# Kernel optimization log

Measured on AMD Instinct MI355X. Metric: run time of the kernel, lower is better.

The kernel has to match this reference:

```python
import jax, jax.numpy as jnp
import numpy as np

B, S, H = 8, 2048, 768
N_SPANS = 512
MAX_SPAN_LEN = 30
WIDTH_VOCAB = 64
N_BIO, N_TYPE, N_SENS = 3, 18, 4
SPAN_DIM = H * 3 + H // 2  # 2688


def setup_inputs() -> dict:
    key = jax.random.key(0)
    ks = jax.random.split(key, 12)
    hidden = jax.random.normal(ks[0], (B, S, H), dtype=jnp.float32)
    # candidate spans: start in [0, S-MAX_SPAN_LEN), width in [1, MAX_SPAN_LEN]
    starts = jax.random.randint(ks[1], (B, N_SPANS), 0, S - MAX_SPAN_LEN)
    widths = jax.random.randint(ks[2], (B, N_SPANS), 1, MAX_SPAN_LEN + 1)
    ends = starts + widths - 1
    candidate_spans = jnp.stack([starts, ends], axis=-1).astype(jnp.int32)  # [B,N,2]
    sc = 0.02
    return {
        "hidden": hidden,
        "candidate_spans": candidate_spans,
        "width_emb": jax.random.normal(ks[3], (WIDTH_VOCAB, H // 2), dtype=jnp.float32) * sc,
        "W_prop": jax.random.normal(ks[4], (H, N_BIO), dtype=jnp.float32) * sc,
        "b_prop": jnp.zeros((N_BIO,), jnp.float32),
        "W_t1": jax.random.normal(ks[5], (SPAN_DIM, H), dtype=jnp.float32) * sc,
        "b_t1": jnp.zeros((H,), jnp.float32),
        "W_t2": jax.random.normal(ks[6], (H, N_TYPE), dtype=jnp.float32) * sc,
        "b_t2": jnp.zeros((N_TYPE,), jnp.float32),
        "W_s1": jax.random.normal(ks[7], (SPAN_DIM + N_TYPE, H), dtype=jnp.float32) * sc,
        "b_s1": jnp.zeros((H,), jnp.float32),
        "W_s2": jax.random.normal(ks[8], (H, N_SENS), dtype=jnp.float32) * sc,
        "b_s2": jnp.zeros((N_SENS,), jnp.float32),
    }


def _span_reprs(hidden, candidate_spans, width_emb):
    # hidden: [B,S,H], candidate_spans: [B,N,2] (all spans valid, 0 <= s <= e < S)
    starts = candidate_spans[..., 0]  # [B,N]
    ends = candidate_spans[..., 1]    # [B,N]
    gather = jax.vmap(lambda h, i: h[i])  # per-batch row gather
    start_h = gather(hidden, starts)  # [B,N,H]
    end_h = gather(hidden, ends)      # [B,N,H]
    # ragged mean-pool via inclusive prefix sums: sum(h[s:e+1]) = P[e+1]-P[s]
    P = jnp.concatenate(
        [jnp.zeros((hidden.shape[0], 1, hidden.shape[2]), hidden.dtype),
         jnp.cumsum(hidden, axis=1)], axis=1)  # [B,S+1,H]
    widths = ends - starts + 1  # [B,N]
    pooled = (gather(P, ends + 1) - gather(P, starts)) / widths[..., None].astype(hidden.dtype)
    width_h = width_emb[jnp.clip(widths, None, WIDTH_VOCAB - 1)]  # [B,N,H//2]
    return jnp.concatenate([start_h, end_h, pooled, width_h], axis=-1)  # [B,N,SPAN_DIM]


def reference(hidden, candidate_spans, width_emb, W_prop, b_prop,
              W_t1, b_t1, W_t2, b_t2, W_s1, b_s1, W_s2, b_s2):
    # proposal head (dropout = identity in eval)
    proposal_logits = hidden @ W_prop + b_prop  # [B,S,3]
    rep = _span_reprs(hidden, candidate_spans, width_emb)  # [B,N,2688]
    t = jax.nn.gelu(rep @ W_t1 + b_t1, approximate=False)
    type_logits = t @ W_t2 + b_t2  # [B,N,18]
    type_probs = jax.nn.softmax(type_logits, axis=-1)
    s_in = jnp.concatenate([rep, type_probs], axis=-1)  # [B,N,2706]
    s = jax.nn.gelu(s_in @ W_s1 + b_s1, approximate=False)
    sensitivity_logits = s @ W_s2 + b_s2  # [B,N,4]
    return proposal_logits, type_logits, sensitivity_logits
```

## Files before the change

### kernel.cpp

```cpp
#include <hip/hip_runtime.h>
#include <hip/hip_bf16.h>
#include <math.h>

#define Bn 8
#define Sn 2048
#define Hn 768
#define NROW 4096
#define SPAN_DIM 2688
#define NBIG 1536
#define NTYPE 18
#define NSENS 4

typedef __attribute__((ext_vector_type(8))) short short8;
typedef __attribute__((ext_vector_type(4))) float floatx4;

__device__ __forceinline__ unsigned short f2bf(float x) {
    __hip_bfloat16 h = __float2bfloat16(x);
    return *reinterpret_cast<unsigned short*>(&h);
}

__device__ __forceinline__ void glds16(const void* g, void* l) {
    __builtin_amdgcn_global_load_lds(
        (const __attribute__((address_space(1))) unsigned int*)g,
        (__attribute__((address_space(3))) unsigned int*)l, 16, 0, 0);
}

__device__ __forceinline__ float gelu_exact(float v) {
    return 0.5f * v * (1.f + erff(v * 0.70710678118654752f));
}

__global__ __launch_bounds__(256) void proposal_kernel(
    const float* __restrict__ hidden, const float* __restrict__ Wp,
    const float* __restrict__ bp, float* __restrict__ out)
{
    int wave = threadIdx.x >> 6;
    int lane = threadIdx.x & 63;
    int row  = blockIdx.x * 4 + wave;
    const float4* h4 = (const float4*)(hidden + (size_t)row * Hn);
    float a0 = 0.f, a1 = 0.f, a2 = 0.f;
#pragma unroll
    for (int i = 0; i < 3; ++i) {
        int kc = i * 64 + lane;
        float4 h = h4[kc];
        const float* w = Wp + kc * 12;
        a0 += h.x * w[0] + h.y * w[3] + h.z * w[6] + h.w * w[9];
        a1 += h.x * w[1] + h.y * w[4] + h.z * w[7] + h.w * w[10];
        a2 += h.x * w[2] + h.y * w[5] + h.z * w[8] + h.w * w[11];
    }
#pragma unroll
    for (int off = 32; off; off >>= 1) {
        a0 += __shfl_xor(a0, off);
        a1 += __shfl_xor(a1, off);
        a2 += __shfl_xor(a2, off);
    }
    if (lane < 3) {
        float v = (lane == 0 ? a0 : (lane == 1 ? a1 : a2)) + bp[lane];
        out[row * 3 + lane] = v;
    }
}

__global__ __launch_bounds__(192) void span_rep_kernel(
    const float* __restrict__ hidden, const int* __restrict__ spans,
    const float* __restrict__ wemb, unsigned short* __restrict__ rep)
{
    int n = blockIdx.x;
    int b = n >> 9;
    int s = spans[n * 2 + 0];
    int e = spans[n * 2 + 1];
    int w = e - s + 1;
    const float4* hb4 = (const float4*)(hidden + (size_t)b * Sn * Hn);
    unsigned short* r = rep + (size_t)n * SPAN_DIM;
    float inv_w = 1.0f / (float)w;
    int tid = threadIdx.x;

    float4 sv = hb4[(size_t)s * 192 + tid];
    float4 ev = hb4[(size_t)e * 192 + tid];
    float4 pv = make_float4(0.f, 0.f, 0.f, 0.f);
    for (int rr = s; rr <= e; ++rr) {
        float4 h = hb4[(size_t)rr * 192 + tid];
        pv.x += h.x; pv.y += h.y; pv.z += h.z; pv.w += h.w;
    }
    pv.x *= inv_w; pv.y *= inv_w; pv.z *= inv_w; pv.w *= inv_w;

    *(ushort4*)&r[tid * 4] =
        make_ushort4(f2bf(sv.x), f2bf(sv.y), f2bf(sv.z), f2bf(sv.w));
    *(ushort4*)&r[Hn + tid * 4] =
        make_ushort4(f2bf(ev.x), f2bf(ev.y), f2bf(ev.z), f2bf(ev.w));
    *(ushort4*)&r[2 * Hn + tid * 4] =
        make_ushort4(f2bf(pv.x), f2bf(pv.y), f2bf(pv.z), f2bf(pv.w));
    if (tid < 96) {
        int wi = w > 63 ? 63 : w;
        float4 wv = ((const float4*)wemb)[wi * 96 + tid];
        *(ushort4*)&r[3 * Hn + tid * 4] =
            make_ushort4(f2bf(wv.x), f2bf(wv.y), f2bf(wv.z), f2bf(wv.w));
    }
}

__global__ __launch_bounds__(256) void transpose_cvt(
    const float* __restrict__ W, unsigned short* __restrict__ Wt,
    int Kin, int N, int ldt)
{
    __shared__ float tile[32][33];
    int k0 = blockIdx.x * 32;
    int n0 = blockIdx.y * 32;
    int tx = threadIdx.x & 31, ty = threadIdx.x >> 5;
#pragma unroll
    for (int i = 0; i < 32; i += 8) {
        int k = k0 + ty + i;
        tile[ty + i][tx] = (k < Kin) ? W[(size_t)k * N + n0 + tx] : 0.f;
    }
    __syncthreads();
#pragma unroll
    for (int i = 0; i < 32; i += 8) {
        int nn = n0 + ty + i;
        Wt[(size_t)nn * ldt + k0 + tx] = f2bf(tile[tx][ty + i]);
    }
}

__global__ __launch_bounds__(256, 3) void gemm_fused(
    const unsigned short* __restrict__ A,
    const unsigned short* __restrict__ Bt,
    const float* __restrict__ bt1, const float* __restrict__ bs1,
    float* __restrict__ obuf)
{
    const int BM = 128, BN = 64, BK = 32;
    __shared__ unsigned short As[BM * BK];
    __shared__ unsigned short Bs[BN * BK];

    int tid = threadIdx.x, wave = tid >> 6, lane = tid & 63;
    int m0 = blockIdx.x * BM, n0 = blockIdx.y * BN;

    int wr = (wave >> 1) * 64;
    int wc = (wave & 1) * 32;
    int fr = lane & 15;
    int fc = lane >> 4;

    int rA0 = tid >> 2,        cA0 = (tid & 3) ^ ((rA0 >> 1) & 3);
    int dA1 = 256 + tid;
    int rA1 = dA1 >> 2,        cA1 = (dA1 & 3) ^ ((rA1 >> 1) & 3);
    int rB  = tid >> 2,        cB  = (tid & 3) ^ ((rB >> 1) & 3);

    const unsigned short* gA0 = A + (size_t)(m0 + rA0) * SPAN_DIM + cA0 * 8;
    const unsigned short* gA1 = A + (size_t)(m0 + rA1) * SPAN_DIM + cA1 * 8;
    const unsigned short* gB  = Bt + (size_t)(n0 + rB) * SPAN_DIM + cB * 8;

    unsigned short* ldsA0 = As + wave * 512;
    unsigned short* ldsA1 = As + 2048 + wave * 512;
    unsigned short* ldsB  = Bs + wave * 512;

    floatx4 acc[4][2] = {};

    for (int k0 = 0; k0 < SPAN_DIM; k0 += BK) {
        glds16(gA0 + k0, ldsA0);
        glds16(gA1 + k0, ldsA1);
        glds16(gB + k0, ldsB);
        __syncthreads();

        short8 af[4], bf[2];
#pragma unroll
        for (int i = 0; i < 4; ++i) {
            int r = wr + i * 16 + fr;
            af[i] = *(const short8*)&As[(r * 4 + (fc ^ ((r >> 1) & 3))) * 8];
        }
#pragma unroll
        for (int i = 0; i < 2; ++i) {
            int r = wc + i * 16 + fr;
            bf[i] = *(const short8*)&Bs[(r * 4 + (fc ^ ((r >> 1) & 3))) * 8];
        }
#pragma unroll
        for (int mi = 0; mi < 4; ++mi)
#pragma unroll
            for (int ni = 0; ni < 2; ++ni)
                acc[mi][ni] = __builtin_amdgcn_mfma_f32_16x16x32_bf16(
                    af[mi], bf[ni], acc[mi][ni], 0, 0, 0);
        __syncthreads();
    }

    bool isT = (n0 < Hn);
    const float* bias = isT ? bt1 : (bs1 - Hn);
    int cr = (lane >> 4) * 4;
#pragma unroll
    for (int mi = 0; mi < 4; ++mi) {
#pragma unroll
        for (int ni = 0; ni < 2; ++ni) {
            int col = n0 + wc + ni * 16 + fr;
            float bv = bias[col];
#pragma unroll
            for (int r = 0; r < 4; ++r) {
                int row = m0 + wr + mi * 16 + cr + r;
                float v = acc[mi][ni][r] + bv;
                if (isT) v = gelu_exact(v);
                obuf[(size_t)row * NBIG + col] = v;
            }
        }
    }
}

__global__ __launch_bounds__(64) void type_head_kernel(
    const float* __restrict__ obuf, const float* __restrict__ W2,
    const float* __restrict__ b2, float* __restrict__ logits_out,
    float* __restrict__ pbuf)
{
    int row = blockIdx.x;
    int lane = threadIdx.x;
    const float* tr = obuf + (size_t)row * NBIG;
    float acc[NTYPE] = {};
#pragma unroll
    for (int i = 0; i < Hn / 64; ++i) {
        int k = lane + i * 64;
        float tv = tr[k];
        const float* wk = W2 + k * NTYPE;
#pragma unroll
        for (int o = 0; o < NTYPE; ++o) acc[o] += tv * wk[o];
    }
#pragma unroll
    for (int o = 0; o < NTYPE; ++o)
#pragma unroll
        for (int off = 32; off; off >>= 1) acc[o] += __shfl_xor(acc[o], off);

    float mx = -1e30f;
#pragma unroll
    for (int o = 0; o < NTYPE; ++o) { acc[o] += b2[o]; mx = fmaxf(mx, acc[o]); }
    float p[NTYPE];
    float sum = 0.f;
#pragma unroll
    for (int o = 0; o < NTYPE; ++o) { p[o] = expf(acc[o] - mx); sum += p[o]; }
    float inv = 1.f / sum;
    if (lane < NTYPE) {
        logits_out[row * NTYPE + lane] = acc[lane];
        pbuf[row * NTYPE + lane] = p[lane] * inv;
    }
}

__global__ __launch_bounds__(64) void tail_sens_kernel(
    const float* __restrict__ obuf, const float* __restrict__ pbuf,
    const float* __restrict__ Ws1, const float* __restrict__ Ws2,
    const float* __restrict__ bs2, float* __restrict__ out)
{
    int row = blockIdx.x;
    int lane = threadIdx.x;
    const float* sp = obuf + (size_t)row * NBIG + Hn;
    float pr[NTYPE];
#pragma unroll
    for (int o = 0; o < NTYPE; ++o) pr[o] = pbuf[row * NTYPE + o];
    float acc[NSENS] = {};
#pragma unroll
    for (int i = 0; i < 12; ++i) {
        int j = lane + i * 64;
        float v = sp[j];
        float t = 0.f;
#pragma unroll
        for (int o = 0; o < NTYPE; ++o)
            t += pr[o] * Ws1[(size_t)(SPAN_DIM + o) * Hn + j];
        v = gelu_exact(v + t);
#pragma unroll
        for (int o = 0; o < NSENS; ++o) acc[o] += v * Ws2[j * NSENS + o];
    }
#pragma unroll
    for (int o = 0; o < NSENS; ++o)
#pragma unroll
        for (int off = 32; off; off >>= 1) acc[o] += __shfl_xor(acc[o], off);
    if (lane < NSENS) out[row * NSENS + lane] = acc[lane] + bs2[lane];
}

extern "C" void kernel_launch(void* const* d_in, const int* in_sizes, int n_in,
                              void* d_out, int out_size, void* d_ws, size_t ws_size,
                              hipStream_t stream)
{
    const float* hidden = (const float*)d_in[0];
    const int*   spans  = (const int*)d_in[1];
    const float* wemb   = (const float*)d_in[2];
    const float* Wp     = (const float*)d_in[3];
    const float* bp     = (const float*)d_in[4];
    const float* Wt1    = (const float*)d_in[5];
    const float* bt1    = (const float*)d_in[6];
    const float* Wt2    = (const float*)d_in[7];
    const float* bt2    = (const float*)d_in[8];
    const float* Ws1    = (const float*)d_in[9];
    const float* bs1    = (const float*)d_in[10];
    const float* Ws2    = (const float*)d_in[11];
    const float* bs2    = (const float*)d_in[12];

    float* out      = (float*)d_out;
    float* out_prop = out;
    float* out_type = out + Bn * Sn * 3;
    float* out_sens = out_type + NROW * NTYPE;

    unsigned short* rep = (unsigned short*)d_ws;
    float* obuf = (float*)(rep + (size_t)NROW * SPAN_DIM);
    unsigned short* WbigT = (unsigned short*)(obuf + (size_t)NROW * NBIG);
    float* pbuf = (float*)(WbigT + (size_t)NBIG * SPAN_DIM);

    transpose_cvt<<<dim3(SPAN_DIM / 32, Hn / 32), 256, 0, stream>>>(
        Wt1, WbigT, SPAN_DIM, Hn, SPAN_DIM);
    transpose_cvt<<<dim3(SPAN_DIM / 32, Hn / 32), 256, 0, stream>>>(
        Ws1, WbigT + (size_t)Hn * SPAN_DIM, SPAN_DIM, Hn, SPAN_DIM);

    proposal_kernel<<<Bn * Sn / 4, 256, 0, stream>>>(hidden, Wp, bp, out_prop);
    span_rep_kernel<<<NROW, 192, 0, stream>>>(hidden, spans, wemb, rep);

    dim3 gg(NROW / 128, NBIG / 64);
    gemm_fused<<<gg, 256, 0, stream>>>(rep, WbigT, bt1, bs1, obuf);

    type_head_kernel<<<NROW, 64, 0, stream>>>(obuf, Wt2, bt2, out_type, pbuf);
    tail_sens_kernel<<<NROW, 64, 0, stream>>>(obuf, pbuf, Ws1, Ws2, bs2, out_sens);
}
```

Baseline: 241.8 us.

## Fuse head kernels, merge weight prep, double GEMM K-tile, unroll span pooling

Merges the two weight transpose launches into one prep kernel that also transposes the small head weights for coalesced access. Fuses the type head and sensitivity tail into one kernel with four rows per block, dropping the probability buffer round trip. Raises the GEMM K-tile from 32 to 64 with a wider swizzle so fewer barriers are paid per K step, at the cost of double the LDS. Unrolls the span mean-pool loop by four with independent accumulators to raise memory-level parallelism.

```diff
diff --git a/kernel.cpp b/kernel.cpp
--- a/kernel.cpp
+++ b/kernel.cpp
@@ -75,12 +75,27 @@
 
     float4 sv = hb4[(size_t)s * 192 + tid];
     float4 ev = hb4[(size_t)e * 192 + tid];
-    float4 pv = make_float4(0.f, 0.f, 0.f, 0.f);
-    for (int rr = s; rr <= e; ++rr) {
+    float4 p0 = make_float4(0.f, 0.f, 0.f, 0.f), p1 = p0, p2 = p0, p3 = p0;
+    int rr = s;
+    for (; rr + 3 <= e; rr += 4) {
+        float4 h0 = hb4[(size_t)(rr + 0) * 192 + tid];
+        float4 h1 = hb4[(size_t)(rr + 1) * 192 + tid];
+        float4 h2 = hb4[(size_t)(rr + 2) * 192 + tid];
+        float4 h3 = hb4[(size_t)(rr + 3) * 192 + tid];
+        p0.x += h0.x; p0.y += h0.y; p0.z += h0.z; p0.w += h0.w;
+        p1.x += h1.x; p1.y += h1.y; p1.z += h1.z; p1.w += h1.w;
+        p2.x += h2.x; p2.y += h2.y; p2.z += h2.z; p2.w += h2.w;
+        p3.x += h3.x; p3.y += h3.y; p3.z += h3.z; p3.w += h3.w;
+    }
+    for (; rr <= e; ++rr) {
         float4 h = hb4[(size_t)rr * 192 + tid];
-        pv.x += h.x; pv.y += h.y; pv.z += h.z; pv.w += h.w;
-    }
-    pv.x *= inv_w; pv.y *= inv_w; pv.z *= inv_w; pv.w *= inv_w;
+        p0.x += h.x; p0.y += h.y; p0.z += h.z; p0.w += h.w;
+    }
+    float4 pv;
+    pv.x = ((p0.x + p1.x) + (p2.x + p3.x)) * inv_w;
+    pv.y = ((p0.y + p1.y) + (p2.y + p3.y)) * inv_w;
+    pv.z = ((p0.z + p1.z) + (p2.z + p3.z)) * inv_w;
+    pv.w = ((p0.w + p1.w) + (p2.w + p3.w)) * inv_w;
 
     *(ushort4*)&r[tid * 4] =
         make_ushort4(f2bf(sv.x), f2bf(sv.y), f2bf(sv.z), f2bf(sv.w));
@@ -96,25 +111,38 @@
     }
 }
 
-__global__ __launch_bounds__(256) void transpose_cvt(
-    const float* __restrict__ W, unsigned short* __restrict__ Wt,
-    int Kin, int N, int ldt)
-{
+__global__ __launch_bounds__(256) void prep_weights(
+    const float* __restrict__ Wt1, const float* __restrict__ Ws1,
+    unsigned short* __restrict__ WbigT,
+    const float* __restrict__ Wt2, const float* __restrict__ Ws2,
+    float* __restrict__ Wt2t, float* __restrict__ Ws2t)
+{
+    int z = blockIdx.z;
+    if (z == 2) {
+        int gid = blockIdx.y * 84 + blockIdx.x;
+        int idx = gid * 256 + threadIdx.x;
+        if (idx < Hn * NTYPE) {
+            int o = idx / Hn, c = idx - o * Hn;
+            Wt2t[idx] = Wt2[c * NTYPE + o];
+        } else if (idx < Hn * (NTYPE + NSENS)) {
+            int j = idx - Hn * NTYPE;
+            int o = j / Hn, c = j - o * Hn;
+            Ws2t[j] = Ws2[c * NSENS + o];
+        }
+        return;
+    }
+    const float* W = (z == 0) ? Wt1 : Ws1;
+    unsigned short* Wt = WbigT + (size_t)z * Hn * SPAN_DIM;
     __shared__ float tile[32][33];
-    int k0 = blockIdx.x * 32;
-    int n0 = blockIdx.y * 32;
+    int k0 = blockIdx.x * 32, n0 = blockIdx.y * 32;
     int tx = threadIdx.x & 31, ty = threadIdx.x >> 5;
 #pragma unroll
-    for (int i = 0; i < 32; i += 8) {
-        int k = k0 + ty + i;
-        tile[ty + i][tx] = (k < Kin) ? W[(size_t)k * N + n0 + tx] : 0.f;
-    }
+    for (int i = 0; i < 32; i += 8)
+        tile[ty + i][tx] = W[(size_t)(k0 + ty + i) * Hn + n0 + tx];
     __syncthreads();
 #pragma unroll
-    for (int i = 0; i < 32; i += 8) {
-        int nn = n0 + ty + i;
-        Wt[(size_t)nn * ldt + k0 + tx] = f2bf(tile[tx][ty + i]);
-    }
+    for (int i = 0; i < 32; i += 8)
+        Wt[(size_t)(n0 + ty + i) * SPAN_DIM + k0 + tx] = f2bf(tile[tx][ty + i]);
 }
 
 __global__ __launch_bounds__(256, 3) void gemm_fused(
@@ -123,56 +151,70 @@
     const float* __restrict__ bt1, const float* __restrict__ bs1,
     float* __restrict__ obuf)
 {
-    const int BM = 128, BN = 64, BK = 32;
-    __shared__ unsigned short As[BM * BK];
-    __shared__ unsigned short Bs[BN * BK];
+    const int BK = 64;
+    __shared__ unsigned short As[128 * BK];
+    __shared__ unsigned short Bs[64 * BK];
 
     int tid = threadIdx.x, wave = tid >> 6, lane = tid & 63;
-    int m0 = blockIdx.x * BM, n0 = blockIdx.y * BN;
-
+    int m0 = blockIdx.x * 128, n0 = blockIdx.y * 64;
     int wr = (wave >> 1) * 64;
     int wc = (wave & 1) * 32;
     int fr = lane & 15;
     int fc = lane >> 4;
 
-    int rA0 = tid >> 2,        cA0 = (tid & 3) ^ ((rA0 >> 1) & 3);
-    int dA1 = 256 + tid;
-    int rA1 = dA1 >> 2,        cA1 = (dA1 & 3) ^ ((rA1 >> 1) & 3);
-    int rB  = tid >> 2,        cB  = (tid & 3) ^ ((rB >> 1) & 3);
-
-    const unsigned short* gA0 = A + (size_t)(m0 + rA0) * SPAN_DIM + cA0 * 8;
-    const unsigned short* gA1 = A + (size_t)(m0 + rA1) * SPAN_DIM + cA1 * 8;
-    const unsigned short* gB  = Bt + (size_t)(n0 + rB) * SPAN_DIM + cB * 8;
-
-    unsigned short* ldsA0 = As + wave * 512;
-    unsigned short* ldsA1 = As + 2048 + wave * 512;
-    unsigned short* ldsB  = Bs + wave * 512;
+    const unsigned short* gA[4];
+#pragma unroll
+    for (int j = 0; j < 4; ++j) {
+        int d = tid + j * 256;
+        int r = d >> 3, c = (d & 7) ^ (r & 7);
+        gA[j] = A + (size_t)(m0 + r) * SPAN_DIM + c * 8;
+    }
+    const unsigned short* gB[2];
+#pragma unroll
+    for (int j = 0; j < 2; ++j) {
+        int d = tid + j * 256;
+        int r = d >> 3, c = (d & 7) ^ (r & 7);
+        gB[j] = Bt + (size_t)(n0 + r) * SPAN_DIM + c * 8;
+    }
+    unsigned short* ldsA[4];
+    unsigned short* ldsB[2];
+#pragma unroll
+    for (int j = 0; j < 4; ++j) ldsA[j] = As + j * 2048 + wave * 512;
+#pragma unroll
+    for (int j = 0; j < 2; ++j) ldsB[j] = Bs + j * 2048 + wave * 512;
 
     floatx4 acc[4][2] = {};
 
     for (int k0 = 0; k0 < SPAN_DIM; k0 += BK) {
-        glds16(gA0 + k0, ldsA0);
-        glds16(gA1 + k0, ldsA1);
-        glds16(gB + k0, ldsB);
+        glds16(gA[0] + k0, ldsA[0]);
+        glds16(gA[1] + k0, ldsA[1]);
+        glds16(gA[2] + k0, ldsA[2]);
+        glds16(gA[3] + k0, ldsA[3]);
+        glds16(gB[0] + k0, ldsB[0]);
+        glds16(gB[1] + k0, ldsB[1]);
         __syncthreads();
 
-        short8 af[4], bf[2];
-#pragma unroll
-        for (int i = 0; i < 4; ++i) {
-            int r = wr + i * 16 + fr;
-            af[i] = *(const short8*)&As[(r * 4 + (fc ^ ((r >> 1) & 3))) * 8];
+#pragma unroll
+        for (int half = 0; half < 2; ++half) {
+            int cb = half * 4 + fc;
+            short8 af[4], bf[2];
+#pragma unroll
+            for (int i = 0; i < 4; ++i) {
+                int r = wr + i * 16 + fr;
+                af[i] = *(const short8*)&As[((r << 3) | (cb ^ (r & 7))) * 8];
+            }
+#pragma unroll
+            for (int i = 0; i < 2; ++i) {
+                int r = wc + i * 16 + fr;
+                bf[i] = *(const short8*)&Bs[((r << 3) | (cb ^ (r & 7))) * 8];
+            }
+#pragma unroll
+            for (int mi = 0; mi < 4; ++mi)
+#pragma unroll
+                for (int ni = 0; ni < 2; ++ni)
+                    acc[mi][ni] = __builtin_amdgcn_mfma_f32_16x16x32_bf16(
+                        af[mi], bf[ni], acc[mi][ni], 0, 0, 0);
         }
-#pragma unroll
-        for (int i = 0; i < 2; ++i) {
-            int r = wc + i * 16 + fr;
-            bf[i] = *(const short8*)&Bs[(r * 4 + (fc ^ ((r >> 1) & 3))) * 8];
-        }
-#pragma unroll
-        for (int mi = 0; mi < 4; ++mi)
-#pragma unroll
-            for (int ni = 0; ni < 2; ++ni)
-                acc[mi][ni] = __builtin_amdgcn_mfma_f32_16x16x32_bf16(
-                    af[mi], bf[ni], acc[mi][ni], 0, 0, 0);
         __syncthreads();
     }
 
@@ -196,22 +238,28 @@
     }
 }
 
-__global__ __launch_bounds__(64) void type_head_kernel(
-    const float* __restrict__ obuf, const float* __restrict__ W2,
-    const float* __restrict__ b2, float* __restrict__ logits_out,
-    float* __restrict__ pbuf)
-{
-    int row = blockIdx.x;
-    int lane = threadIdx.x;
+__global__ __launch_bounds__(256) void heads_kernel(
+    const float* __restrict__ obuf, const float* __restrict__ Wt2t,
+    const float* __restrict__ bt2, const float* __restrict__ Ws1,
+    const float* __restrict__ Ws2t, const float* __restrict__ bs2,
+    float* __restrict__ out_type, float* __restrict__ out_sens)
+{
+    int wave = threadIdx.x >> 6, lane = threadIdx.x & 63;
+    int row = blockIdx.x * 4 + wave;
     const float* tr = obuf + (size_t)row * NBIG;
-    float acc[NTYPE] = {};
-#pragma unroll
-    for (int i = 0; i < Hn / 64; ++i) {
-        int k = lane + i * 64;
-        float tv = tr[k];
-        const float* wk = W2 + k * NTYPE;
-#pragma unroll
-        for (int o = 0; o < NTYPE; ++o) acc[o] += tv * wk[o];
+
+    float t[12];
+#pragma unroll
+    for (int i = 0; i < 12; ++i) t[i] = tr[lane + i * 64];
+
+    float acc[NTYPE];
+#pragma unroll
+    for (int o = 0; o < NTYPE; ++o) {
+        const float* w = Wt2t + o * Hn + lane;
+        float a = 0.f;
+#pragma unroll
+        for (int i = 0; i < 12; ++i) a += t[i] * w[i * 64];
+        acc[o] = a;
     }
 #pragma unroll
     for (int o = 0; o < NTYPE; ++o)
@@ -220,47 +268,38 @@
 
     float mx = -1e30f;
 #pragma unroll
-    for (int o = 0; o < NTYPE; ++o) { acc[o] += b2[o]; mx = fmaxf(mx, acc[o]); }
-    float p[NTYPE];
-    float sum = 0.f;
-#pragma unroll
-    for (int o = 0; o < NTYPE; ++o) { p[o] = expf(acc[o] - mx); sum += p[o]; }
+    for (int o = 0; o < NTYPE; ++o) { acc[o] += bt2[o]; mx = fmaxf(mx, acc[o]); }
+#pragma unroll
+    for (int o = 0; o < NTYPE; ++o)
+        if (lane == o) out_type[row * NTYPE + o] = acc[o];
+
+    float pr[NTYPE], sum = 0.f;
+#pragma unroll
+    for (int o = 0; o < NTYPE; ++o) { pr[o] = expf(acc[o] - mx); sum += pr[o]; }
     float inv = 1.f / sum;
-    if (lane < NTYPE) {
-        logits_out[row * NTYPE + lane] = acc[lane];
-        pbuf[row * NTYPE + lane] = p[lane] * inv;
-    }
-}
-
-__global__ __launch_bounds__(64) void tail_sens_kernel(
-    const float* __restrict__ obuf, const float* __restrict__ pbuf,
-    const float* __restrict__ Ws1, const float* __restrict__ Ws2,
-    const float* __restrict__ bs2, float* __restrict__ out)
-{
-    int row = blockIdx.x;
-    int lane = threadIdx.x;
-    const float* sp = obuf + (size_t)row * NBIG + Hn;
-    float pr[NTYPE];
-#pragma unroll
-    for (int o = 0; o < NTYPE; ++o) pr[o] = pbuf[row * NTYPE + o];
-    float acc[NSENS] = {};
+#pragma unroll
+    for (int o = 0; o < NTYPE; ++o) pr[o] *= inv;
+
+    const float* sp = tr + Hn;
+    const float* Wtail = Ws1 + (size_t)SPAN_DIM * Hn;
+    float acc2[NSENS] = {};
 #pragma unroll
     for (int i = 0; i < 12; ++i) {
-        int j = lane + i * 64;
-        float v = sp[j];
-        float t = 0.f;
-#pragma unroll
-        for (int o = 0; o < NTYPE; ++o)
-            t += pr[o] * Ws1[(size_t)(SPAN_DIM + o) * Hn + j];
-        v = gelu_exact(v + t);
-#pragma unroll
-        for (int o = 0; o < NSENS; ++o) acc[o] += v * Ws2[j * NSENS + o];
+        int c = lane + i * 64;
+        float tl = 0.f;
+#pragma unroll
+        for (int o = 0; o < NTYPE; ++o) tl += pr[o] * Wtail[o * Hn + c];
+        float v = gelu_exact(sp[c] + tl);
+#pragma unroll
+        for (int o = 0; o < NSENS; ++o) acc2[o] += v * Ws2t[o * Hn + c];
     }
 #pragma unroll
     for (int o = 0; o < NSENS; ++o)
 #pragma unroll
-        for (int off = 32; off; off >>= 1) acc[o] += __shfl_xor(acc[o], off);
-    if (lane < NSENS) out[row * NSENS + lane] = acc[lane] + bs2[lane];
+        for (int off = 32; off; off >>= 1) acc2[o] += __shfl_xor(acc2[o], off);
+#pragma unroll
+    for (int o = 0; o < NSENS; ++o)
+        if (lane == o) out_sens[row * NSENS + o] = acc2[o] + bs2[o];
 }
 
 extern "C" void kernel_launch(void* const* d_in, const int* in_sizes, int n_in,
@@ -289,12 +328,11 @@
     unsigned short* rep = (unsigned short*)d_ws;
     float* obuf = (float*)(rep + (size_t)NROW * SPAN_DIM);
     unsigned short* WbigT = (unsigned short*)(obuf + (size_t)NROW * NBIG);
-    float* pbuf = (float*)(WbigT + (size_t)NBIG * SPAN_DIM);
-
-    transpose_cvt<<<dim3(SPAN_DIM / 32, Hn / 32), 256, 0, stream>>>(
-        Wt1, WbigT, SPAN_DIM, Hn, SPAN_DIM);
-    transpose_cvt<<<dim3(SPAN_DIM / 32, Hn / 32), 256, 0, stream>>>(
-        Ws1, WbigT + (size_t)Hn * SPAN_DIM, SPAN_DIM, Hn, SPAN_DIM);
+    float* Wt2t = (float*)(WbigT + (size_t)NBIG * SPAN_DIM);
+    float* Ws2t = Wt2t + NTYPE * Hn;
+
+    prep_weights<<<dim3(SPAN_DIM / 32, Hn / 32, 3), 256, 0, stream>>>(
+        Wt1, Ws1, WbigT, Wt2, Ws2, Wt2t, Ws2t);
 
     proposal_kernel<<<Bn * Sn / 4, 256, 0, stream>>>(hidden, Wp, bp, out_prop);
     span_rep_kernel<<<NROW, 192, 0, stream>>>(hidden, spans, wemb, rep);
@@ -302,6 +340,6 @@
     dim3 gg(NROW / 128, NBIG / 64);
     gemm_fused<<<gg, 256, 0, stream>>>(rep, WbigT, bt1, bs1, obuf);
 
-    type_head_kernel<<<NROW, 64, 0, stream>>>(obuf, Wt2, bt2, out_type, pbuf);
-    tail_sens_kernel<<<NROW, 64, 0, stream>>>(obuf, pbuf, Ws1, Ws2, bs2, out_sens);
-}
+    heads_kernel<<<NROW / 4, 256, 0, stream>>>(
+        obuf, Wt2t, bt2, Ws1, Ws2t, bs2, out_type, out_sens);
+}
```

Result: faster. 227.3 us (-6.0%).
